# Performance work log

Measured on AMD Instinct MI355X. Metric: run time of the kernel, lower is better.

Reference implementation:

```python
import jax, jax.numpy as jnp
import numpy as np
from jax.ops import segment_sum

N_NODES = 100000
N_EDGES = 1600000
N_GRAPHS = 2048
VOCAB = 1000
EMBED = 64
HID = 64
N_CL = 2


def setup_inputs() -> dict:
    key = jax.random.key(0)
    ks = jax.random.split(key, 9)
    x = jax.random.randint(ks[0], (N_NODES,), 0, VOCAB)
    edge_index = jax.random.randint(ks[1], (2, N_EDGES), 0, N_NODES)
    batch = jnp.sort(jax.random.randint(ks[2], (N_NODES,), 0, N_GRAPHS))
    emb = jax.random.normal(ks[3], (VOCAB, EMBED), dtype=jnp.float32)
    emb = emb.at[0].set(0.0)  # padding_idx=0
    s1 = 1.0 / np.sqrt(EMBED)
    s2 = 1.0 / np.sqrt(HID)
    W1 = jax.random.uniform(ks[4], (EMBED, HID), jnp.float32, -s1, s1)
    b1 = jnp.zeros((HID,), jnp.float32)
    W2 = jax.random.uniform(ks[5], (HID, HID), jnp.float32, -s2, s2)
    b2 = jnp.zeros((HID,), jnp.float32)
    Wl = jax.random.uniform(ks[6], (HID, N_CL), jnp.float32, -s2, s2)
    bl = jax.random.uniform(ks[7], (N_CL,), jnp.float32, -s2, s2)
    return {"x": x, "edge_index": edge_index, "batch": batch,
            "emb": emb, "W1": W1, "b1": b1, "W2": W2, "b2": b2,
            "Wl": Wl, "bl": bl}


def _gcn_conv(h, row, col, norm, W, b):
    # h: [N, Fin] -> [N, Fout]; PyG GCNConv: lin -> gather -> norm -> scatter-add -> bias
    h = h @ W
    msg = h[row] * norm[:, None]          # [E+N, Fout] gathered, normalized messages
    out = segment_sum(msg, col, num_segments=N_NODES)
    return out + b


def reference(x, edge_index, batch, emb, W1, b1, W2, b2, Wl, bl):
    # add self loops (GCNConv default)
    loop = jnp.arange(N_NODES)
    row = jnp.concatenate([edge_index[0], loop])  # sources
    col = jnp.concatenate([edge_index[1], loop])  # targets
    # symmetric normalization: deg^{-1/2}[row] * deg^{-1/2}[col]
    deg = segment_sum(jnp.ones_like(col, dtype=jnp.float32), col, num_segments=N_NODES)
    dinv = jnp.where(deg > 0, jax.lax.rsqrt(jnp.maximum(deg, 1.0)), 0.0)
    norm = dinv[row] * dinv[col]

    h = emb[x]                                        # [N, EMBED]
    h = jax.nn.relu(_gcn_conv(h, row, col, norm, W1, b1))
    h = jax.nn.relu(_gcn_conv(h, row, col, norm, W2, b2))

    # global mean pool over graphs
    sums = segment_sum(h, batch, num_segments=N_GRAPHS)          # [G, HID]
    cnts = segment_sum(jnp.ones((N_NODES,), jnp.float32), batch, num_segments=N_GRAPHS)
    pooled = sums / jnp.maximum(cnts, 1.0)[:, None]
    return pooled @ Wl + bl                                      # [G, N_CL]
```

## Files before the change

### kernel.cpp

```cpp
#include <hip/hip_runtime.h>
#include <hip/hip_fp16.h>

#define N_NODES  100000
#define N_EDGES  1600000
#define N_GRAPHS 2048
#define VOCAB    1000
#define EMBED    64
#define HID      64
#define N_CL     2
#define CAP      64
#define NBLK     391
#define EBLK     6250
#define VBLK     63
#define NSWEEP   8
#define RANGE    12500

typedef __half2 h2;

__device__ inline uint2 pack_h4(float4 a) {
    h2 lo = __float22half2_rn(make_float2(a.x, a.y));
    h2 hi = __float22half2_rn(make_float2(a.z, a.w));
    uint2 r;
    r.x = *reinterpret_cast<unsigned*>(&lo);
    r.y = *reinterpret_cast<unsigned*>(&hi);
    return r;
}

__device__ inline void acc_h8(h2 acc[4], uint4 raw) {
    acc[0] = __hadd2(acc[0], *reinterpret_cast<h2*>(&raw.x));
    acc[1] = __hadd2(acc[1], *reinterpret_cast<h2*>(&raw.y));
    acc[2] = __hadd2(acc[2], *reinterpret_cast<h2*>(&raw.z));
    acc[3] = __hadd2(acc[3], *reinterpret_cast<h2*>(&raw.w));
}

__device__ inline void h8_to_f(const h2 acc[4], float4& A, float4& B) {
    float2 f0 = __half22float2(acc[0]);
    float2 f1 = __half22float2(acc[1]);
    float2 f2 = __half22float2(acc[2]);
    float2 f3 = __half22float2(acc[3]);
    A.x = f0.x; A.y = f0.y; A.z = f1.x; A.w = f1.y;
    B.x = f2.x; B.y = f2.y; B.z = f3.x; B.w = f3.y;
}

__device__ inline void xor_reduce8(float4& A, float4& B) {
#pragma unroll
    for (int m = 8; m <= 32; m <<= 1) {
        A.x += __shfl_xor(A.x, m, 64); A.y += __shfl_xor(A.y, m, 64);
        A.z += __shfl_xor(A.z, m, 64); A.w += __shfl_xor(A.w, m, 64);
        B.x += __shfl_xor(B.x, m, 64); B.y += __shfl_xor(B.y, m, 64);
        B.z += __shfl_xor(B.z, m, 64); B.w += __shfl_xor(B.w, m, 64);
    }
}

__global__ __launch_bounds__(256) void k_fill_slots(const int* __restrict__ row, const int* __restrict__ col,
                                                    int* __restrict__ cnt, int* __restrict__ slots,
                                                    const int* __restrict__ batch, int* __restrict__ start,
                                                    const float* __restrict__ emb, const float* __restrict__ W1,
                                                    float* __restrict__ E) {
    int bid = blockIdx.x;
    if (bid < NSWEEP * EBLK) {
        int sweep = bid & (NSWEEP - 1);
        int e = (bid >> 3) * 256 + threadIdx.x;
        int c = col[e];
        if ((unsigned)(c - sweep * RANGE) < (unsigned)RANGE) {
            int pos = atomicAdd(&cnt[c], 1);
            if (pos < CAP) slots[c * CAP + pos] = row[e];
        }
    } else if (bid < NSWEEP * EBLK + NBLK) {
        int v = (bid - NSWEEP * EBLK) * 256 + threadIdx.x;
        if (v >= N_NODES) return;
        int b = batch[v];
        int pb = (v == 0) ? -1 : batch[v - 1];
        for (int g = pb + 1; g <= b; ++g) start[g] = v;
        if (v == N_NODES - 1)
            for (int g = b + 1; g <= N_GRAPHS; ++g) start[g] = N_NODES;
    } else {
        int t = (bid - NSWEEP * EBLK - NBLK) * 256 + threadIdx.x;
        int j = t >> 4;
        int f4 = t & 15;
        if (j >= VOCAB) return;
        const float4* W4 = (const float4*)W1;
        const float* er = emb + j * EMBED;
        float4 acc = make_float4(0.f, 0.f, 0.f, 0.f);
#pragma unroll 8
        for (int k = 0; k < EMBED; ++k) {
            float hv = er[k];
            float4 w = W4[k * 16 + f4];
            acc.x += hv * w.x; acc.y += hv * w.y; acc.z += hv * w.z; acc.w += hv * w.w;
        }
        ((float4*)E)[t] = acc;
    }
}

__global__ __launch_bounds__(256) void k_tn1(const int* __restrict__ x, const int* __restrict__ cnt,
                                             const float* __restrict__ E, uint2* __restrict__ tn) {
    int t = blockIdx.x * 256 + threadIdx.x;
    int v = t >> 4;
    int f4 = t & 15;
    float d = rsqrtf((float)(cnt[v] + 1));
    float4 a = ((const float4*)E)[x[v] * 16 + f4];
    a.x *= d; a.y *= d; a.z *= d; a.w *= d;
    tn[t] = pack_h4(a);
}

__global__ __launch_bounds__(256) void k_agg_gemm(const uint4* __restrict__ tn,
                                                  const int* __restrict__ cnt,
                                                  const int* __restrict__ slots,
                                                  const float* __restrict__ bias,
                                                  const float* __restrict__ W2,
                                                  __half* __restrict__ tn2) {
    __shared__ float hrow[8][HID];
    int wid = threadIdx.x >> 6;
    int lane = threadIdx.x & 63;
    int fg = lane & 7;
    int es = lane >> 3;
    int v0 = blockIdx.x * 8 + wid * 2;
    int v1 = v0 + 1;
    int c0 = cnt[v0], c1 = cnt[v1];
    int n0 = min(c0, CAP), n1 = min(c1, CAP);
    const int* sl0 = slots + v0 * CAP;
    const int* sl1 = slots + v1 * CAP;
    h2 z = __float2half2_rn(0.f);
    h2 a0[4] = {z, z, z, z};
    h2 a1[4] = {z, z, z, z};
    if (es == 0) acc_h8(a0, tn[v0 * 8 + fg]);
    if (es == 1) acc_h8(a1, tn[v1 * 8 + fg]);
    int m = max(n0, n1);
    int i = 0;
    for (; i + 16 <= m; i += 16) {
        int ia = i + es, ib = i + 8 + es;
        if (ia < n0) { uint4 r = tn[sl0[ia] * 8 + fg]; acc_h8(a0, r); }
        if (ia < n1) { uint4 r = tn[sl1[ia] * 8 + fg]; acc_h8(a1, r); }
        if (ib < n0) { uint4 r = tn[sl0[ib] * 8 + fg]; acc_h8(a0, r); }
        if (ib < n1) { uint4 r = tn[sl1[ib] * 8 + fg]; acc_h8(a1, r); }
    }
    for (; i < m; i += 8) {
        int ia = i + es;
        if (ia < n0) { uint4 r = tn[sl0[ia] * 8 + fg]; acc_h8(a0, r); }
        if (ia < n1) { uint4 r = tn[sl1[ia] * 8 + fg]; acc_h8(a1, r); }
    }
    float4 a0A, a0B, a1A, a1B;
    h8_to_f(a0, a0A, a0B);
    h8_to_f(a1, a1A, a1B);
    xor_reduce8(a0A, a0B);
    xor_reduce8(a1A, a1B);
    float d0 = rsqrtf((float)(c0 + 1));
    float d1 = rsqrtf((float)(c1 + 1));
    float4 bA = ((const float4*)bias)[fg * 2 + 0];
    float4 bB = ((const float4*)bias)[fg * 2 + 1];
    if (es == 0) {
        float4 oA, oB;
        oA.x = fmaxf(d0 * a0A.x + bA.x, 0.f); oA.y = fmaxf(d0 * a0A.y + bA.y, 0.f);
        oA.z = fmaxf(d0 * a0A.z + bA.z, 0.f); oA.w = fmaxf(d0 * a0A.w + bA.w, 0.f);
        oB.x = fmaxf(d0 * a0B.x + bB.x, 0.f); oB.y = fmaxf(d0 * a0B.y + bB.y, 0.f);
        oB.z = fmaxf(d0 * a0B.z + bB.z, 0.f); oB.w = fmaxf(d0 * a0B.w + bB.w, 0.f);
        ((float4*)&hrow[wid * 2][fg * 8])[0] = oA;
        ((float4*)&hrow[wid * 2][fg * 8])[1] = oB;
    }
    if (es == 1) {
        float4 oA, oB;
        oA.x = fmaxf(d1 * a1A.x + bA.x, 0.f); oA.y = fmaxf(d1 * a1A.y + bA.y, 0.f);
        oA.z = fmaxf(d1 * a1A.z + bA.z, 0.f); oA.w = fmaxf(d1 * a1A.w + bA.w, 0.f);
        oB.x = fmaxf(d1 * a1B.x + bB.x, 0.f); oB.y = fmaxf(d1 * a1B.y + bB.y, 0.f);
        oB.z = fmaxf(d1 * a1B.z + bB.z, 0.f); oB.w = fmaxf(d1 * a1B.w + bB.w, 0.f);
        ((float4*)&hrow[wid * 2 + 1][fg * 8])[0] = oA;
        ((float4*)&hrow[wid * 2 + 1][fg * 8])[1] = oB;
    }
    __syncthreads();
    const float* hr0 = hrow[wid * 2];
    const float* hr1 = hrow[wid * 2 + 1];
    float s0 = 0.f, s1 = 0.f;
#pragma unroll 8
    for (int k = 0; k < HID; ++k) {
        float w = W2[k * HID + lane];
        s0 += hr0[k] * w;
        s1 += hr1[k] * w;
    }
    tn2[v0 * HID + lane] = __float2half(d0 * s0);
    tn2[v1 * HID + lane] = __float2half(d1 * s1);
}

__global__ __launch_bounds__(256) void k_agg(const uint4* __restrict__ tn,
                                             const int* __restrict__ cnt,
                                             const int* __restrict__ slots,
                                             const float* __restrict__ bias,
                                             float* __restrict__ h) {
    int wid = threadIdx.x >> 6;
    int lane = threadIdx.x & 63;
    int fg = lane & 7;
    int es = lane >> 3;
    int v0 = blockIdx.x * 8 + wid * 2;
    int v1 = v0 + 1;
    int c0 = cnt[v0], c1 = cnt[v1];
    int n0 = min(c0, CAP), n1 = min(c1, CAP);
    const int* sl0 = slots + v0 * CAP;
    const int* sl1 = slots + v1 * CAP;
    h2 z = __float2half2_rn(0.f);
    h2 a0[4] = {z, z, z, z};
    h2 a1[4] = {z, z, z, z};
    if (es == 0) acc_h8(a0, tn[v0 * 8 + fg]);
    if (es == 1) acc_h8(a1, tn[v1 * 8 + fg]);
    int m = max(n0, n1);
    int i = 0;
    for (; i + 16 <= m; i += 16) {
        int ia = i + es, ib = i + 8 + es;
        if (ia < n0) { uint4 r = tn[sl0[ia] * 8 + fg]; acc_h8(a0, r); }
        if (ia < n1) { uint4 r = tn[sl1[ia] * 8 + fg]; acc_h8(a1, r); }
        if (ib < n0) { uint4 r = tn[sl0[ib] * 8 + fg]; acc_h8(a0, r); }
        if (ib < n1) { uint4 r = tn[sl1[ib] * 8 + fg]; acc_h8(a1, r); }
    }
    for (; i < m; i += 8) {
        int ia = i + es;
        if (ia < n0) { uint4 r = tn[sl0[ia] * 8 + fg]; acc_h8(a0, r); }
        if (ia < n1) { uint4 r = tn[sl1[ia] * 8 + fg]; acc_h8(a1, r); }
    }
    float4 a0A, a0B, a1A, a1B;
    h8_to_f(a0, a0A, a0B);
    h8_to_f(a1, a1A, a1B);
    xor_reduce8(a0A, a0B);
    xor_reduce8(a1A, a1B);
    float4 bA = ((const float4*)bias)[fg * 2 + 0];
    float4 bB = ((const float4*)bias)[fg * 2 + 1];
    if (es == 0) {
        float d0 = rsqrtf((float)(c0 + 1));
        float4 oA, oB;
        oA.x = fmaxf(d0 * a0A.x + bA.x, 0.f); oA.y = fmaxf(d0 * a0A.y + bA.y, 0.f);
        oA.z = fmaxf(d0 * a0A.z + bA.z, 0.f); oA.w = fmaxf(d0 * a0A.w + bA.w, 0.f);
        oB.x = fmaxf(d0 * a0B.x + bB.x, 0.f); oB.y = fmaxf(d0 * a0B.y + bB.y, 0.f);
        oB.z = fmaxf(d0 * a0B.z + bB.z, 0.f); oB.w = fmaxf(d0 * a0B.w + bB.w, 0.f);
        ((float4*)&h[v0 * HID + fg * 8])[0] = oA;
        ((float4*)&h[v0 * HID + fg * 8])[1] = oB;
    }
    if (es == 1) {
        float d1 = rsqrtf((float)(c1 + 1));
        float4 oA, oB;
        oA.x = fmaxf(d1 * a1A.x + bA.x, 0.f); oA.y = fmaxf(d1 * a1A.y + bA.y, 0.f);
        oA.z = fmaxf(d1 * a1A.z + bA.z, 0.f); oA.w = fmaxf(d1 * a1A.w + bA.w, 0.f);
        oB.x = fmaxf(d1 * a1B.x + bB.x, 0.f); oB.y = fmaxf(d1 * a1B.y + bB.y, 0.f);
        oB.z = fmaxf(d1 * a1B.z + bB.z, 0.f); oB.w = fmaxf(d1 * a1B.w + bB.w, 0.f);
        ((float4*)&h[v1 * HID + fg * 8])[0] = oA;
        ((float4*)&h[v1 * HID + fg * 8])[1] = oB;
    }
}

__global__ __launch_bounds__(256) void k_pool_out(const float* __restrict__ h,
                                                  const int* __restrict__ start,
                                                  const float* __restrict__ Wl,
                                                  const float* __restrict__ bl,
                                                  float* __restrict__ out) {
    int g = (blockIdx.x * 256 + threadIdx.x) >> 6;
    int f = threadIdx.x & 63;
    if (g >= N_GRAPHS) return;
    int s = start[g], e = start[g + 1];
    float acc = 0.f;
    int v = s;
    for (; v + 4 <= e; v += 4) {
        float a0 = h[(v + 0) * HID + f];
        float a1 = h[(v + 1) * HID + f];
        float a2 = h[(v + 2) * HID + f];
        float a3 = h[(v + 3) * HID + f];
        acc += (a0 + a1) + (a2 + a3);
    }
    for (; v < e; ++v) acc += h[v * HID + f];
    float m = acc / fmaxf((float)(e - s), 1.f);
    float p0 = m * Wl[f * N_CL + 0];
    float p1 = m * Wl[f * N_CL + 1];
#pragma unroll
    for (int off = 32; off > 0; off >>= 1) {
        p0 += __shfl_down(p0, off, 64);
        p1 += __shfl_down(p1, off, 64);
    }
    if (f == 0) {
        out[g * N_CL + 0] = p0 + bl[0];
        out[g * N_CL + 1] = p1 + bl[1];
    }
}

extern "C" void kernel_launch(void* const* d_in, const int* in_sizes, int n_in,
                              void* d_out, int out_size, void* d_ws, size_t ws_size,
                              hipStream_t stream) {
    const int*   x     = (const int*)d_in[0];
    const int*   ei    = (const int*)d_in[1];
    const int*   batch = (const int*)d_in[2];
    const float* emb   = (const float*)d_in[3];
    const float* W1    = (const float*)d_in[4];
    const float* b1    = (const float*)d_in[5];
    const float* W2    = (const float*)d_in[6];
    const float* b2    = (const float*)d_in[7];
    const float* Wl    = (const float*)d_in[8];
    const float* bl    = (const float*)d_in[9];
    float* out = (float*)d_out;

    const int* row = ei;
    const int* col = ei + N_EDGES;

    char* ws = (char*)d_ws;
    size_t off = 0;
    auto alloc = [&](size_t bytes) { char* p = ws + off; off = (off + bytes + 511) & ~(size_t)511; return p; };
    const size_t FEAT_BYTES  = (size_t)N_NODES * HID * sizeof(float);
    const size_t FEATH_BYTES = (size_t)N_NODES * HID * sizeof(__half);
    float* A      = (float*)alloc(FEAT_BYTES);
    __half* Bt    = (__half*)alloc(FEATH_BYTES);
    int*   slots  = (int*)  alloc((size_t)N_NODES * CAP * sizeof(int));
    float* E      = (float*)alloc((size_t)VOCAB * HID * sizeof(float));
    int*   start  = (int*)  alloc((size_t)(N_GRAPHS + 1) * sizeof(int));
    int*   cnt    = (int*)  alloc((size_t)N_NODES * sizeof(int));

    dim3 blk(256);
    dim3 g_fill(NSWEEP * EBLK + NBLK + VBLK);
    dim3 g_tn1(N_NODES * 16 / 256);
    dim3 g_agg(N_NODES / 8);
    dim3 g_po((N_GRAPHS * 64 + 255) / 256);

    hipMemsetAsync(cnt, 0, (size_t)N_NODES * sizeof(int), stream);

    k_fill_slots<<<g_fill, blk, 0, stream>>>(row, col, cnt, slots, batch, start, emb, W1, E);

    k_tn1<<<g_tn1, blk, 0, stream>>>(x, cnt, E, (uint2*)A);

    k_agg_gemm<<<g_agg, blk, 0, stream>>>((const uint4*)A, cnt, slots, b1, W2, Bt);

    k_agg<<<g_agg, blk, 0, stream>>>((const uint4*)Bt, cnt, slots, b2, A);

    k_pool_out<<<g_po, blk, 0, stream>>>(A, start, Wl, bl, out);
}
```

Baseline: 271.4 us.

## Fuse all stages into one persistent cooperative kernel with grid syncs

Replaces the memset plus five separate kernel launches with a single cooperative persistent kernel. It loops over virtual blocks for each stage (zeroing, graph starts, embedding GEMM, edge slot fill, first features, two aggregations, pooling) and separates stages with grid.sync(). The goal is to remove launch overhead and inter-kernel gaps. In exchange, a grid capped at 2048 blocks must cover every stage, and each grid barrier has a cost. The original multi-kernel path is kept as a fallback if the cooperative launch fails.

```diff
diff --git a/kernel.cpp b/kernel.cpp
--- a/kernel.cpp
+++ b/kernel.cpp
@@ -1,5 +1,8 @@
 #include <hip/hip_runtime.h>
 #include <hip/hip_fp16.h>
+#include <hip/hip_cooperative_groups.h>
+
+namespace cg = cooperative_groups;
 
 #define N_NODES  100000
 #define N_EDGES  1600000
@@ -15,6 +18,14 @@
 #define NSWEEP   8
 #define RANGE    12500
 
+#define ZT    391
+#define GBT   391
+#define ET    63
+#define FILLT 50000
+#define TN1T  6250
+#define AGGT  12500
+#define POOLT 512
+
 typedef __half2 h2;
 
 __device__ inline uint2 pack_h4(float4 a) {
@@ -49,6 +60,219 @@
         A.z += __shfl_xor(A.z, m, 64); A.w += __shfl_xor(A.w, m, 64);
         B.x += __shfl_xor(B.x, m, 64); B.y += __shfl_xor(B.y, m, 64);
         B.z += __shfl_xor(B.z, m, 64); B.w += __shfl_xor(B.w, m, 64);
+    }
+}
+
+template <bool WRITE_H>
+__device__ inline void agg_two(const uint4* __restrict__ tn, const int* __restrict__ cnt,
+                               const int* __restrict__ slots, const float* __restrict__ bias,
+                               int v0, int lane, int wid,
+                               float* __restrict__ hlds, float* __restrict__ hglob,
+                               float& d0_out, float& d1_out) {
+    int fg = lane & 7;
+    int es = lane >> 3;
+    int v1 = v0 + 1;
+    int c0 = cnt[v0], c1 = cnt[v1];
+    int n0 = min(c0, CAP), n1 = min(c1, CAP);
+    const int* sl0 = slots + v0 * CAP;
+    const int* sl1 = slots + v1 * CAP;
+    h2 z = __float2half2_rn(0.f);
+    h2 a0[4] = {z, z, z, z};
+    h2 a1[4] = {z, z, z, z};
+    if (es == 0) acc_h8(a0, tn[v0 * 8 + fg]);
+    if (es == 1) acc_h8(a1, tn[v1 * 8 + fg]);
+    int m = max(n0, n1);
+    int i = 0;
+    for (; i + 16 <= m; i += 16) {
+        int ia = i + es, ib = i + 8 + es;
+        if (ia < n0) { uint4 r = tn[sl0[ia] * 8 + fg]; acc_h8(a0, r); }
+        if (ia < n1) { uint4 r = tn[sl1[ia] * 8 + fg]; acc_h8(a1, r); }
+        if (ib < n0) { uint4 r = tn[sl0[ib] * 8 + fg]; acc_h8(a0, r); }
+        if (ib < n1) { uint4 r = tn[sl1[ib] * 8 + fg]; acc_h8(a1, r); }
+    }
+    for (; i < m; i += 8) {
+        int ia = i + es;
+        if (ia < n0) { uint4 r = tn[sl0[ia] * 8 + fg]; acc_h8(a0, r); }
+        if (ia < n1) { uint4 r = tn[sl1[ia] * 8 + fg]; acc_h8(a1, r); }
+    }
+    float4 a0A, a0B, a1A, a1B;
+    h8_to_f(a0, a0A, a0B);
+    h8_to_f(a1, a1A, a1B);
+    xor_reduce8(a0A, a0B);
+    xor_reduce8(a1A, a1B);
+    float d0 = rsqrtf((float)(c0 + 1));
+    float d1 = rsqrtf((float)(c1 + 1));
+    d0_out = d0; d1_out = d1;
+    float4 bA = ((const float4*)bias)[fg * 2 + 0];
+    float4 bB = ((const float4*)bias)[fg * 2 + 1];
+    if (es == 0) {
+        float4 oA, oB;
+        oA.x = fmaxf(d0 * a0A.x + bA.x, 0.f); oA.y = fmaxf(d0 * a0A.y + bA.y, 0.f);
+        oA.z = fmaxf(d0 * a0A.z + bA.z, 0.f); oA.w = fmaxf(d0 * a0A.w + bA.w, 0.f);
+        oB.x = fmaxf(d0 * a0B.x + bB.x, 0.f); oB.y = fmaxf(d0 * a0B.y + bB.y, 0.f);
+        oB.z = fmaxf(d0 * a0B.z + bB.z, 0.f); oB.w = fmaxf(d0 * a0B.w + bB.w, 0.f);
+        float* dst = WRITE_H ? (hglob + v0 * HID + fg * 8) : (hlds + (wid * 2) * HID + fg * 8);
+        ((float4*)dst)[0] = oA;
+        ((float4*)dst)[1] = oB;
+    }
+    if (es == 1) {
+        float4 oA, oB;
+        oA.x = fmaxf(d1 * a1A.x + bA.x, 0.f); oA.y = fmaxf(d1 * a1A.y + bA.y, 0.f);
+        oA.z = fmaxf(d1 * a1A.z + bA.z, 0.f); oA.w = fmaxf(d1 * a1A.w + bA.w, 0.f);
+        oB.x = fmaxf(d1 * a1B.x + bB.x, 0.f); oB.y = fmaxf(d1 * a1B.y + bB.y, 0.f);
+        oB.z = fmaxf(d1 * a1B.z + bB.z, 0.f); oB.w = fmaxf(d1 * a1B.w + bB.w, 0.f);
+        float* dst = WRITE_H ? (hglob + v1 * HID + fg * 8) : (hlds + (wid * 2 + 1) * HID + fg * 8);
+        ((float4*)dst)[0] = oA;
+        ((float4*)dst)[1] = oB;
+    }
+}
+
+__global__ __launch_bounds__(256, 8) void k_mega(const int* __restrict__ x,
+                                                 const int* __restrict__ row,
+                                                 const int* __restrict__ col,
+                                                 const int* __restrict__ batch,
+                                                 const float* __restrict__ emb,
+                                                 const float* __restrict__ W1,
+                                                 const float* __restrict__ b1,
+                                                 const float* __restrict__ W2,
+                                                 const float* __restrict__ b2,
+                                                 const float* __restrict__ Wl,
+                                                 const float* __restrict__ bl,
+                                                 float* __restrict__ out,
+                                                 int* __restrict__ cnt,
+                                                 int* __restrict__ slots,
+                                                 int* __restrict__ start,
+                                                 float* __restrict__ E,
+                                                 uint2* __restrict__ tn1,
+                                                 __half* __restrict__ tn2,
+                                                 float* __restrict__ h) {
+    cg::grid_group grid = cg::this_grid();
+    __shared__ float hrow[8][HID];
+    int bid = blockIdx.x;
+    int tid = threadIdx.x;
+    int gstride = gridDim.x;
+
+    for (int t = bid; t < ZT + GBT + ET; t += gstride) {
+        if (t < ZT) {
+            int v = t * 256 + tid;
+            if (v < N_NODES) cnt[v] = 0;
+        } else if (t < ZT + GBT) {
+            int v = (t - ZT) * 256 + tid;
+            if (v < N_NODES) {
+                int b = batch[v];
+                int pb = (v == 0) ? -1 : batch[v - 1];
+                for (int g = pb + 1; g <= b; ++g) start[g] = v;
+                if (v == N_NODES - 1)
+                    for (int g = b + 1; g <= N_GRAPHS; ++g) start[g] = N_NODES;
+            }
+        } else {
+            int tt = (t - ZT - GBT) * 256 + tid;
+            int j = tt >> 4;
+            int f4 = tt & 15;
+            if (j < VOCAB) {
+                const float4* W4 = (const float4*)W1;
+                const float* er = emb + j * EMBED;
+                float4 acc = make_float4(0.f, 0.f, 0.f, 0.f);
+#pragma unroll 8
+                for (int k = 0; k < EMBED; ++k) {
+                    float hv = er[k];
+                    float4 w = W4[k * 16 + f4];
+                    acc.x += hv * w.x; acc.y += hv * w.y; acc.z += hv * w.z; acc.w += hv * w.w;
+                }
+                ((float4*)E)[tt] = acc;
+            }
+        }
+    }
+    grid.sync();
+
+    for (int t = bid; t < FILLT; t += gstride) {
+        int sweep = t & (NSWEEP - 1);
+        int e = (t >> 3) * 256 + tid;
+        int c = col[e];
+        if ((unsigned)(c - sweep * RANGE) < (unsigned)RANGE) {
+            int pos = atomicAdd(&cnt[c], 1);
+            if (pos < CAP) slots[c * CAP + pos] = row[e];
+        }
+    }
+    grid.sync();
+
+    for (int t = bid; t < TN1T; t += gstride) {
+        int tt = t * 256 + tid;
+        int v = tt >> 4;
+        int f4 = tt & 15;
+        float d = rsqrtf((float)(cnt[v] + 1));
+        float4 a = ((const float4*)E)[x[v] * 16 + f4];
+        a.x *= d; a.y *= d; a.z *= d; a.w *= d;
+        tn1[tt] = pack_h4(a);
+    }
+    grid.sync();
+
+    {
+        int wid = tid >> 6;
+        int lane = tid & 63;
+        for (int t = bid; t < AGGT; t += gstride) {
+            int v0 = t * 8 + wid * 2;
+            float d0, d1;
+            agg_two<false>((const uint4*)tn1, cnt, slots, b1, v0, lane, wid,
+                           &hrow[0][0], nullptr, d0, d1);
+            __syncthreads();
+            const float* hr0 = &hrow[wid * 2][0];
+            const float* hr1 = &hrow[wid * 2 + 1][0];
+            float s0 = 0.f, s1 = 0.f;
+#pragma unroll 8
+            for (int k = 0; k < HID; ++k) {
+                float w = W2[k * HID + lane];
+                s0 += hr0[k] * w;
+                s1 += hr1[k] * w;
+            }
+            tn2[v0 * HID + lane] = __float2half(d0 * s0);
+            tn2[(v0 + 1) * HID + lane] = __float2half(d1 * s1);
+            __syncthreads();
+        }
+    }
+    grid.sync();
+
+    {
+        int wid = tid >> 6;
+        int lane = tid & 63;
+        for (int t = bid; t < AGGT; t += gstride) {
+            int v0 = t * 8 + wid * 2;
+            float d0, d1;
+            agg_two<true>((const uint4*)tn2, cnt, slots, b2, v0, lane, wid,
+                          nullptr, h, d0, d1);
+        }
+    }
+    grid.sync();
+
+    {
+        int wid = tid >> 6;
+        int f = tid & 63;
+        for (int t = bid; t < POOLT; t += gstride) {
+            int g = t * 4 + wid;
+            int s = start[g], e = start[g + 1];
+            float acc = 0.f;
+            int v = s;
+            for (; v + 4 <= e; v += 4) {
+                float a0 = h[(v + 0) * HID + f];
+                float a1 = h[(v + 1) * HID + f];
+                float a2 = h[(v + 2) * HID + f];
+                float a3 = h[(v + 3) * HID + f];
+                acc += (a0 + a1) + (a2 + a3);
+            }
+            for (; v < e; ++v) acc += h[v * HID + f];
+            float mn = acc / fmaxf((float)(e - s), 1.f);
+            float p0 = mn * Wl[f * N_CL + 0];
+            float p1 = mn * Wl[f * N_CL + 1];
+#pragma unroll
+            for (int o = 32; o > 0; o >>= 1) {
+                p0 += __shfl_down(p0, o, 64);
+                p1 += __shfl_down(p1, o, 64);
+            }
+            if (f == 0) {
+                out[g * N_CL + 0] = p0 + bl[0];
+                out[g * N_CL + 1] = p1 + bl[1];
+            }
+        }
     }
 }
 
@@ -112,63 +336,12 @@
     __shared__ float hrow[8][HID];
     int wid = threadIdx.x >> 6;
     int lane = threadIdx.x & 63;
-    int fg = lane & 7;
-    int es = lane >> 3;
     int v0 = blockIdx.x * 8 + wid * 2;
-    int v1 = v0 + 1;
-    int c0 = cnt[v0], c1 = cnt[v1];
-    int n0 = min(c0, CAP), n1 = min(c1, CAP);
-    const int* sl0 = slots + v0 * CAP;
-    const int* sl1 = slots + v1 * CAP;
-    h2 z = __float2half2_rn(0.f);
-    h2 a0[4] = {z, z, z, z};
-    h2 a1[4] = {z, z, z, z};
-    if (es == 0) acc_h8(a0, tn[v0 * 8 + fg]);
-    if (es == 1) acc_h8(a1, tn[v1 * 8 + fg]);
-    int m = max(n0, n1);
-    int i = 0;
-    for (; i + 16 <= m; i += 16) {
-        int ia = i + es, ib = i + 8 + es;
-        if (ia < n0) { uint4 r = tn[sl0[ia] * 8 + fg]; acc_h8(a0, r); }
-        if (ia < n1) { uint4 r = tn[sl1[ia] * 8 + fg]; acc_h8(a1, r); }
-        if (ib < n0) { uint4 r = tn[sl0[ib] * 8 + fg]; acc_h8(a0, r); }
-        if (ib < n1) { uint4 r = tn[sl1[ib] * 8 + fg]; acc_h8(a1, r); }
-    }
-    for (; i < m; i += 8) {
-        int ia = i + es;
-        if (ia < n0) { uint4 r = tn[sl0[ia] * 8 + fg]; acc_h8(a0, r); }
-        if (ia < n1) { uint4 r = tn[sl1[ia] * 8 + fg]; acc_h8(a1, r); }
-    }
-    float4 a0A, a0B, a1A, a1B;
-    h8_to_f(a0, a0A, a0B);
-    h8_to_f(a1, a1A, a1B);
-    xor_reduce8(a0A, a0B);
-    xor_reduce8(a1A, a1B);
-    float d0 = rsqrtf((float)(c0 + 1));
-    float d1 = rsqrtf((float)(c1 + 1));
-    float4 bA = ((const float4*)bias)[fg * 2 + 0];
-    float4 bB = ((const float4*)bias)[fg * 2 + 1];
-    if (es == 0) {
-        float4 oA, oB;
-        oA.x = fmaxf(d0 * a0A.x + bA.x, 0.f); oA.y = fmaxf(d0 * a0A.y + bA.y, 0.f);
-        oA.z = fmaxf(d0 * a0A.z + bA.z, 0.f); oA.w = fmaxf(d0 * a0A.w + bA.w, 0.f);
-        oB.x = fmaxf(d0 * a0B.x + bB.x, 0.f); oB.y = fmaxf(d0 * a0B.y + bB.y, 0.f);
-        oB.z = fmaxf(d0 * a0B.z + bB.z, 0.f); oB.w = fmaxf(d0 * a0B.w + bB.w, 0.f);
-        ((float4*)&hrow[wid * 2][fg * 8])[0] = oA;
-        ((float4*)&hrow[wid * 2][fg * 8])[1] = oB;
-    }
-    if (es == 1) {
-        float4 oA, oB;
-        oA.x = fmaxf(d1 * a1A.x + bA.x, 0.f); oA.y = fmaxf(d1 * a1A.y + bA.y, 0.f);
-        oA.z = fmaxf(d1 * a1A.z + bA.z, 0.f); oA.w = fmaxf(d1 * a1A.w + bA.w, 0.f);
-        oB.x = fmaxf(d1 * a1B.x + bB.x, 0.f); oB.y = fmaxf(d1 * a1B.y + bB.y, 0.f);
-        oB.z = fmaxf(d1 * a1B.z + bB.z, 0.f); oB.w = fmaxf(d1 * a1B.w + bB.w, 0.f);
-        ((float4*)&hrow[wid * 2 + 1][fg * 8])[0] = oA;
-        ((float4*)&hrow[wid * 2 + 1][fg * 8])[1] = oB;
-    }
+    float d0, d1;
+    agg_two<false>(tn, cnt, slots, bias, v0, lane, wid, &hrow[0][0], nullptr, d0, d1);
     __syncthreads();
-    const float* hr0 = hrow[wid * 2];
-    const float* hr1 = hrow[wid * 2 + 1];
+    const float* hr0 = &hrow[wid * 2][0];
+    const float* hr1 = &hrow[wid * 2 + 1][0];
     float s0 = 0.f, s1 = 0.f;
 #pragma unroll 8
     for (int k = 0; k < HID; ++k) {
@@ -177,7 +350,7 @@
         s1 += hr1[k] * w;
     }
     tn2[v0 * HID + lane] = __float2half(d0 * s0);
-    tn2[v1 * HID + lane] = __float2half(d1 * s1);
+    tn2[(v0 + 1) * HID + lane] = __float2half(d1 * s1);
 }
 
 __global__ __launch_bounds__(256) void k_agg(const uint4* __restrict__ tn,
@@ -187,60 +360,9 @@
                                              float* __restrict__ h) {
     int wid = threadIdx.x >> 6;
     int lane = threadIdx.x & 63;
-    int fg = lane & 7;
-    int es = lane >> 3;
     int v0 = blockIdx.x * 8 + wid * 2;
-    int v1 = v0 + 1;
-    int c0 = cnt[v0], c1 = cnt[v1];
-    int n0 = min(c0, CAP), n1 = min(c1, CAP);
-    const int* sl0 = slots + v0 * CAP;
-    const int* sl1 = slots + v1 * CAP;
-    h2 z = __float2half2_rn(0.f);
-    h2 a0[4] = {z, z, z, z};
-    h2 a1[4] = {z, z, z, z};
-    if (es == 0) acc_h8(a0, tn[v0 * 8 + fg]);
-    if (es == 1) acc_h8(a1, tn[v1 * 8 + fg]);
-    int m = max(n0, n1);
-    int i = 0;
-    for (; i + 16 <= m; i += 16) {
-        int ia = i + es, ib = i + 8 + es;
-        if (ia < n0) { uint4 r = tn[sl0[ia] * 8 + fg]; acc_h8(a0, r); }
-        if (ia < n1) { uint4 r = tn[sl1[ia] * 8 + fg]; acc_h8(a1, r); }
-        if (ib < n0) { uint4 r = tn[sl0[ib] * 8 + fg]; acc_h8(a0, r); }
-        if (ib < n1) { uint4 r = tn[sl1[ib] * 8 + fg]; acc_h8(a1, r); }
-    }
-    for (; i < m; i += 8) {
-        int ia = i + es;
-        if (ia < n0) { uint4 r = tn[sl0[ia] * 8 + fg]; acc_h8(a0, r); }
-        if (ia < n1) { uint4 r = tn[sl1[ia] * 8 + fg]; acc_h8(a1, r); }
-    }
-    float4 a0A, a0B, a1A, a1B;
-    h8_to_f(a0, a0A, a0B);
-    h8_to_f(a1, a1A, a1B);
-    xor_reduce8(a0A, a0B);
-    xor_reduce8(a1A, a1B);
-    float4 bA = ((const float4*)bias)[fg * 2 + 0];
-    float4 bB = ((const float4*)bias)[fg * 2 + 1];
-    if (es == 0) {
-        float d0 = rsqrtf((float)(c0 + 1));
-        float4 oA, oB;
-        oA.x = fmaxf(d0 * a0A.x + bA.x, 0.f); oA.y = fmaxf(d0 * a0A.y + bA.y, 0.f);
-        oA.z = fmaxf(d0 * a0A.z + bA.z, 0.f); oA.w = fmaxf(d0 * a0A.w + bA.w, 0.f);
-        oB.x = fmaxf(d0 * a0B.x + bB.x, 0.f); oB.y = fmaxf(d0 * a0B.y + bB.y, 0.f);
-        oB.z = fmaxf(d0 * a0B.z + bB.z, 0.f); oB.w = fmaxf(d0 * a0B.w + bB.w, 0.f);
-        ((float4*)&h[v0 * HID + fg * 8])[0] = oA;
-        ((float4*)&h[v0 * HID + fg * 8])[1] = oB;
-    }
-    if (es == 1) {
-        float d1 = rsqrtf((float)(c1 + 1));
-        float4 oA, oB;
-        oA.x = fmaxf(d1 * a1A.x + bA.x, 0.f); oA.y = fmaxf(d1 * a1A.y + bA.y, 0.f);
-        oA.z = fmaxf(d1 * a1A.z + bA.z, 0.f); oA.w = fmaxf(d1 * a1A.w + bA.w, 0.f);
-        oB.x = fmaxf(d1 * a1B.x + bB.x, 0.f); oB.y = fmaxf(d1 * a1B.y + bB.y, 0.f);
-        oB.z = fmaxf(d1 * a1B.z + bB.z, 0.f); oB.w = fmaxf(d1 * a1B.w + bB.w, 0.f);
-        ((float4*)&h[v1 * HID + fg * 8])[0] = oA;
-        ((float4*)&h[v1 * HID + fg * 8])[1] = oB;
-    }
+    float d0, d1;
+    agg_two<true>(tn, cnt, slots, bias, v0, lane, wid, nullptr, h, d0, d1);
 }
 
 __global__ __launch_bounds__(256) void k_pool_out(const float* __restrict__ h,
@@ -299,28 +421,53 @@
     auto alloc = [&](size_t bytes) { char* p = ws + off; off = (off + bytes + 511) & ~(size_t)511; return p; };
     const size_t FEAT_BYTES  = (size_t)N_NODES * HID * sizeof(float);
     const size_t FEATH_BYTES = (size_t)N_NODES * HID * sizeof(__half);
-    float* A      = (float*)alloc(FEAT_BYTES);
+    float*  A     = (float*)alloc(FEAT_BYTES);
     __half* Bt    = (__half*)alloc(FEATH_BYTES);
     int*   slots  = (int*)  alloc((size_t)N_NODES * CAP * sizeof(int));
     float* E      = (float*)alloc((size_t)VOCAB * HID * sizeof(float));
     int*   start  = (int*)  alloc((size_t)(N_GRAPHS + 1) * sizeof(int));
     int*   cnt    = (int*)  alloc((size_t)N_NODES * sizeof(int));
 
-    dim3 blk(256);
-    dim3 g_fill(NSWEEP * EBLK + NBLK + VBLK);
-    dim3 g_tn1(N_NODES * 16 / 256);
-    dim3 g_agg(N_NODES / 8);
-    dim3 g_po((N_GRAPHS * 64 + 255) / 256);
-
-    hipMemsetAsync(cnt, 0, (size_t)N_NODES * sizeof(int), stream);
-
-    k_fill_slots<<<g_fill, blk, 0, stream>>>(row, col, cnt, slots, batch, start, emb, W1, E);
-
-    k_tn1<<<g_tn1, blk, 0, stream>>>(x, cnt, E, (uint2*)A);
-
-    k_agg_gemm<<<g_agg, blk, 0, stream>>>((const uint4*)A, cnt, slots, b1, W2, Bt);
-
-    k_agg<<<g_agg, blk, 0, stream>>>((const uint4*)Bt, cnt, slots, b2, A);
-
-    k_pool_out<<<g_po, blk, 0, stream>>>(A, start, Wl, bl, out);
-}
+    uint2*  tn1 = (uint2*)A;
+    float*  h   = A;
+
+    int occ = 0;
+    hipError_t qerr = hipOccupancyMaxActiveBlocksPerMultiprocessor(&occ, k_mega, 256, 0);
+    int ncu = 0;
+    hipError_t derr = hipDeviceGetAttribute(&ncu, hipDeviceAttributeMultiprocessorCount, 0);
+    int grid = 0;
+    if (qerr == hipSuccess && derr == hipSuccess && occ > 0 && ncu > 0) {
+        long long g = (long long)occ * ncu;
+        if (g > 2048) g = 2048;
+        grid = (int)(g & ~7LL);
+    }
+
+    bool coop_ok = false;
+    if (grid >= 1024) {
+        void* args[] = {
+            (void*)&x, (void*)&row, (void*)&col, (void*)&batch,
+            (void*)&emb, (void*)&W1, (void*)&b1, (void*)&W2, (void*)&b2,
+            (void*)&Wl, (void*)&bl, (void*)&out,
+            (void*)&cnt, (void*)&slots, (void*)&start, (void*)&E,
+            (void*)&tn1, (void*)&Bt, (void*)&h
+        };
+        hipError_t lerr = hipLaunchCooperativeKernel((const void*)k_mega, dim3(grid), dim3(256),
+                                                     args, 0, stream);
+        coop_ok = (lerr == hipSuccess);
+    }
+
+    if (!coop_ok) {
+        dim3 blk(256);
+        dim3 g_fill(NSWEEP * EBLK + NBLK + VBLK);
+        dim3 g_tn1(N_NODES * 16 / 256);
+        dim3 g_agg(N_NODES / 8);
+        dim3 g_po((N_GRAPHS * 64 + 255) / 256);
+
+        hipMemsetAsync(cnt, 0, (size_t)N_NODES * sizeof(int), stream);
+        k_fill_slots<<<g_fill, blk, 0, stream>>>(row, col, cnt, slots, batch, start, emb, W1, E);
+        k_tn1<<<g_tn1, blk, 0, stream>>>(x, cnt, E, tn1);
+        k_agg_gemm<<<g_agg, blk, 0, stream>>>((const uint4*)tn1, cnt, slots, b1, W2, Bt);
+        k_agg<<<g_agg, blk, 0, stream>>>((const uint4*)Bt, cnt, slots, b2, h);
+        k_pool_out<<<g_po, blk, 0, stream>>>(h, start, Wl, bl, out);
+    }
+}
```

Result: slower. 906.4 us (+234.0%).
